# Optimization experiments

Hardware: AMD Instinct MI355X
Metric: run time of the kernel (lower is better)

The kernel has to match this reference:

```python
import jax, jax.numpy as jnp
import numpy as np

B, K, N = 8, 4, 131072
DENSITY = 0.3
NEG_PAD = -1000.0
NEG_IDLE = -1.0e8


def setup_inputs() -> dict:
    rng = np.random.default_rng(0)
    mask_s = rng.random((B, K, N)) < DENSITY  # bool, per-slot variable counts
    mask_a = rng.random((B, K, N)) < DENSITY
    ts = int(mask_s.sum())
    ta = int(mask_a.sum())
    key = jax.random.key(0)
    k1, k2, k3, k4 = jax.random.split(key, 4)
    return {
        "rgb": jax.random.normal(k1, (ts, 3), dtype=jnp.float32),
        "logits_surface": jax.random.normal(k2, (ts, 1), dtype=jnp.float32),
        "logits_air": jax.random.normal(k3, (ta, 1), dtype=jnp.float32),
        "idle_states": (jax.random.uniform(k4, (B, K)) < 0.25).astype(jnp.float32),
        "mask_eval_surface": jnp.asarray(mask_s),
        "mask_eval_air": jnp.asarray(mask_a),
    }


def _expand(mask, values):
    # mask: (B,K,N) bool; values: (total, C) packed in row-major (b,k,n) mask order.
    # Returns (B,K,N,C) where masked positions hold their packed value (others garbage,
    # to be overwritten by the caller's jnp.where). Equivalent to the torch B*K scatter loop.
    m = mask.reshape(-1)
    pos = jnp.cumsum(m.astype(jnp.int32)) - 1  # packed index for each masked slot
    pos = jnp.clip(pos, 0, values.shape[0] - 1)
    return jnp.take(values, pos, axis=0).reshape(mask.shape + (values.shape[-1],))


def reference(rgb, logits_surface, logits_air, idle_states,
              mask_eval_surface, mask_eval_air):
    alive = (1.0 - idle_states)[:, :, None, None]  # (B,K,1,1)
    idle = idle_states[:, :, None, None]
    ms = mask_eval_surface[..., None]  # (B,K,N,1)
    ma = mask_eval_air[..., None]

    rgb_out = jnp.where(ms, _expand(mask_eval_surface, rgb) * alive, 0.0)
    logits_surface_out = jnp.where(
        ms, _expand(mask_eval_surface, logits_surface) * alive + idle * NEG_IDLE, NEG_PAD)
    logits_air_out = jnp.where(
        ma, _expand(mask_eval_air, logits_air) * alive + idle * NEG_IDLE, NEG_PAD)
    return rgb_out, logits_surface_out, logits_air_out
```

## Files before the change

kernel.cpp:

```cpp
#include <hip/hip_runtime.h>
#include <stdint.h>

#define NTOT      4194304LL
#define CHUNK     2048
#define NBLK      2048
#define NEG_PAD   (-1000.0f)
#define NEG_IDLE  (-100000000.0f)
#define CAPS      832
#define CAPA      832

typedef unsigned long long u64;
typedef float float3u __attribute__((ext_vector_type(3), aligned(4)));
typedef float float4a __attribute__((ext_vector_type(4), aligned(16)));
typedef int   int4v   __attribute__((ext_vector_type(4), aligned(16)));

__global__ __launch_bounds__(256, 8) void count_kernel(
    const int* __restrict__ ms, const int* __restrict__ ma,
    unsigned short* __restrict__ cmp, u64* __restrict__ totals)
{
    const int t = threadIdx.x, lane = t & 63, wave = t >> 6;
    const unsigned bid = blockIdx.x;
    const long long base = (long long)bid * CHUNK;

    const int4v* ms4 = (const int4v*)(ms + base);
    const int4v* ma4 = (const int4v*)(ma + base);
    int4v s0 = __builtin_nontemporal_load(ms4 + 2 * t);
    int4v s1 = __builtin_nontemporal_load(ms4 + 2 * t + 1);
    int4v a0 = __builtin_nontemporal_load(ma4 + 2 * t);
    int4v a1 = __builtin_nontemporal_load(ma4 + 2 * t + 1);
    unsigned sbits = (unsigned)(s0[0] != 0)        | ((unsigned)(s0[1] != 0) << 1)
                   | ((unsigned)(s0[2] != 0) << 2) | ((unsigned)(s0[3] != 0) << 3)
                   | ((unsigned)(s1[0] != 0) << 4) | ((unsigned)(s1[1] != 0) << 5)
                   | ((unsigned)(s1[2] != 0) << 6) | ((unsigned)(s1[3] != 0) << 7);
    unsigned abits = (unsigned)(a0[0] != 0)        | ((unsigned)(a0[1] != 0) << 1)
                   | ((unsigned)(a0[2] != 0) << 2) | ((unsigned)(a0[3] != 0) << 3)
                   | ((unsigned)(a1[0] != 0) << 4) | ((unsigned)(a1[1] != 0) << 5)
                   | ((unsigned)(a1[2] != 0) << 6) | ((unsigned)(a1[3] != 0) << 7);

    cmp[bid * 256u + (unsigned)t] = (unsigned short)(sbits | (abits << 8));

    unsigned cnt = __popc(sbits) | (__popc(abits) << 16);
    #pragma unroll
    for (int o = 32; o; o >>= 1) cnt += __shfl_down(cnt, o, 64);
    __shared__ unsigned lds[4];
    if (lane == 0) lds[wave] = cnt;
    __syncthreads();
    if (t == 0) {
        unsigned tot = lds[0] + lds[1] + lds[2] + lds[3];
        totals[bid] = (u64)(tot & 0xffffu) | ((u64)(tot >> 16) << 32);
    }
}

__global__ __launch_bounds__(256, 5) void expand_kernel(
    const float* __restrict__ rgb, const float* __restrict__ lsurf,
    const float* __restrict__ lair, const float* __restrict__ idle,
    const unsigned short* __restrict__ cmp, const u64* __restrict__ totals,
    unsigned rgb_max, unsigned ts_max, unsigned ta_max,
    float* __restrict__ out_rgb, float* __restrict__ out_ls, float* __restrict__ out_la)
{
    __shared__ unsigned wsum[4];
    __shared__ u64 wacc[4];
    __shared__ unsigned packLDS[256];
    __shared__ unsigned prefLDS[256];
    __shared__ float    rgbLDS[3072];
    __shared__ float    rgbSrc[CAPS * 3];
    __shared__ float    lsS[CAPS];
    __shared__ float    laS[CAPA];

    const int t = threadIdx.x, lane = t & 63, wave = t >> 6;
    const unsigned bid = blockIdx.x;
    const long long base = (long long)bid * CHUNK;

    unsigned pk = cmp[bid * 256u + (unsigned)t];
    u64 acc = 0;
    #pragma unroll
    for (int j = 0; j < 8; ++j) {
        unsigned idx = (unsigned)t * 8u + (unsigned)j;
        acc += (idx < bid) ? totals[idx] : 0ULL;
    }
    const float idle_v = idle[(int)(base >> 17)];

    packLDS[t] = pk;
    unsigned cnt = __popc(pk & 0xffu) | (__popc(pk >> 8) << 16);

    unsigned x = cnt;
    #pragma unroll
    for (int o = 1; o < 64; o <<= 1) {
        unsigned y = __shfl_up(x, o, 64);
        if (lane >= o) x += y;
    }
    if (lane == 63) wsum[wave] = x;
    #pragma unroll
    for (int o = 32; o; o >>= 1) acc += __shfl_down(acc, o, 64);
    if (lane == 0) wacc[wave] = acc;
    __syncthreads();
    unsigned pre = (wave > 0 ? wsum[0] : 0u) + (wave > 1 ? wsum[1] : 0u)
                 + (wave > 2 ? wsum[2] : 0u);
    prefLDS[t] = pre + x - cnt;
    u64 basesum = wacc[0] + wacc[1] + wacc[2] + wacc[3];
    const unsigned excS = (unsigned)(basesum & 0xffffffffULL);
    const unsigned excA = (unsigned)(basesum >> 32);
    unsigned totPk = wsum[0] + wsum[1] + wsum[2] + wsum[3];
    const unsigned totS = totPk & 0xffffu;
    const unsigned totA = totPk >> 16;

    {
        const unsigned nS = totS < CAPS ? totS : CAPS;
        const unsigned nA = totA < CAPA ? totA : CAPA;
        const float* rgbB = rgb + 3LL * excS;
        const float* lsB  = lsurf + excS;
        const float* laB  = lair + excA;
        for (unsigned i = t; i < nS * 3u; i += 256u) rgbSrc[i] = rgbB[i];
        for (unsigned i = t; i < nS; i += 256u)      lsS[i]   = lsB[i];
        for (unsigned i = t; i < nA; i += 256u)      laS[i]   = laB[i];
    }
    __syncthreads();

    const float alive     = 1.0f - idle_v;
    const float idle_term = idle_v * NEG_IDLE;
    const int  sub = t >> 3, b = t & 7;
    const unsigned bm = (1u << b) - 1u;
    const int  hp = t >> 1;
    const unsigned nib = (unsigned)(t & 1) * 4u;
    const unsigned nm  = (1u << nib) - 1u;

    #pragma unroll
    for (int h = 0; h < 2; ++h) {
        #pragma unroll
        for (int r = 0; r < 4; ++r) {
            const int g = h * 4 + r;
            const int p = (g << 5) + sub;
            unsigned w  = packLDS[p];
            unsigned pv = prefLDS[p];
            const int li = r * 768 + 3 * t;
            if ((w >> b) & 1u) {
                unsigned lr = (pv & 0xffffu) + __popc(w & bm);
                float vx, vy, vz;
                if (lr < CAPS) {
                    vx = rgbSrc[3 * lr]; vy = rgbSrc[3 * lr + 1]; vz = rgbSrc[3 * lr + 2];
                } else {
                    unsigned pr = excS + lr; pr = pr < rgb_max ? pr : rgb_max;
                    float3u v = *(const float3u*)(rgb + 3LL * pr);
                    vx = v.x; vy = v.y; vz = v.z;
                }
                rgbLDS[li]     = vx * alive;
                rgbLDS[li + 1] = vy * alive;
                rgbLDS[li + 2] = vz * alive;
            } else {
                rgbLDS[li] = 0.f; rgbLDS[li + 1] = 0.f; rgbLDS[li + 2] = 0.f;
            }
        }
        {
            const int p = h * 128 + hp;
            unsigned w  = packLDS[p];
            unsigned pv = prefLDS[p];
            unsigned ws = w & 0xffu, wa = (w >> 8) & 0xffu;
            unsigned baseS = (pv & 0xffffu) + __popc(ws & nm);
            unsigned baseA = (pv >> 16)     + __popc(wa & nm);
            unsigned sb = (ws >> nib) & 0xFu;
            unsigned ab = (wa >> nib) & 0xFu;
            float lsv[4], lav[4];
            #pragma unroll
            for (int j = 0; j < 4; ++j) {
                unsigned mj = (1u << j) - 1u;
                unsigned rs = baseS + __popc(sb & mj);
                float vs = rs < CAPS ? lsS[rs]
                         : lsurf[(excS + rs) < ts_max ? (excS + rs) : ts_max];
                lsv[j] = ((sb >> j) & 1u) ? vs * alive + idle_term : NEG_PAD;
                unsigned ra = baseA + __popc(ab & mj);
                float va = ra < CAPA ? laS[ra]
                         : lair[(excA + ra) < ta_max ? (excA + ra) : ta_max];
                lav[j] = ((ab >> j) & 1u) ? va * alive + idle_term : NEG_PAD;
            }
            const long long eb = base + h * 1024 + 4 * t;
            float4a vls; vls.x = lsv[0]; vls.y = lsv[1]; vls.z = lsv[2]; vls.w = lsv[3];
            float4a vla; vla.x = lav[0]; vla.y = lav[1]; vla.z = lav[2]; vla.w = lav[3];
            __builtin_nontemporal_store(vls, (float4a*)(out_ls + eb));
            __builtin_nontemporal_store(vla, (float4a*)(out_la + eb));
        }
        __syncthreads();
        float4a* dst = (float4a*)(out_rgb + 3 * base) + h * 768;
        const float4a* src = (const float4a*)rgbLDS;
        __builtin_nontemporal_store(src[t],       dst + t);
        __builtin_nontemporal_store(src[t + 256], dst + t + 256);
        __builtin_nontemporal_store(src[t + 512], dst + t + 512);
        __syncthreads();
    }
}

extern "C" void kernel_launch(void* const* d_in, const int* in_sizes, int n_in,
                              void* d_out, int out_size, void* d_ws, size_t ws_size,
                              hipStream_t stream)
{
    const float* rgb   = (const float*)d_in[0];
    const float* lsurf = (const float*)d_in[1];
    const float* lair  = (const float*)d_in[2];
    const float* idle  = (const float*)d_in[3];
    const int*   ms    = (const int*)d_in[4];
    const int*   ma    = (const int*)d_in[5];

    unsigned rgb_max = (unsigned)(in_sizes[0] / 3 - 1);
    unsigned ts_max  = (unsigned)(in_sizes[1] - 1);
    unsigned ta_max  = (unsigned)(in_sizes[2] - 1);

    float* out     = (float*)d_out;
    float* out_rgb = out;
    float* out_ls  = out + NTOT * 3;
    float* out_la  = out_ls + NTOT;

    u64* totals = (u64*)d_ws;
    unsigned short* cmp = (unsigned short*)((char*)d_ws + 16384);

    count_kernel<<<NBLK, 256, 0, stream>>>(ms, ma, cmp, totals);
    expand_kernel<<<NBLK, 256, 0, stream>>>(rgb, lsurf, lair, idle, cmp, totals,
                                            rgb_max, ts_max, ta_max,
                                            out_rgb, out_ls, out_la);
}
```

Before: 150.0 us.

## Drop rgb LDS staging, vectorize aligned source loads, raise expand occupancy

Removes the rgbLDS transpose buffer and writes rgb outputs directly as strided scalar nontemporal stores, dropping two barriers per half. Source preloads into LDS now use aligned float4 nontemporal loads with head offset and tail handling. LDS caches shrink to 768 entries and launch bounds rise to 8 blocks per SM to improve occupancy. The trade-off is less coalesced rgb stores and more fallback global reads when a chunk exceeds the smaller cap.

```diff
diff --git a/kernel.cpp b/kernel.cpp
--- a/kernel.cpp
+++ b/kernel.cpp
@@ -6,8 +6,8 @@
 #define NBLK      2048
 #define NEG_PAD   (-1000.0f)
 #define NEG_IDLE  (-100000000.0f)
-#define CAPS      832
-#define CAPA      832
+#define CAPS      768
+#define CAPA      768
 
 typedef unsigned long long u64;
 typedef float float3u __attribute__((ext_vector_type(3), aligned(4)));
@@ -51,7 +51,7 @@
     }
 }
 
-__global__ __launch_bounds__(256, 5) void expand_kernel(
+__global__ __launch_bounds__(256, 8) void expand_kernel(
     const float* __restrict__ rgb, const float* __restrict__ lsurf,
     const float* __restrict__ lair, const float* __restrict__ idle,
     const unsigned short* __restrict__ cmp, const u64* __restrict__ totals,
@@ -62,10 +62,12 @@
     __shared__ u64 wacc[4];
     __shared__ unsigned packLDS[256];
     __shared__ unsigned prefLDS[256];
-    __shared__ float    rgbLDS[3072];
-    __shared__ float    rgbSrc[CAPS * 3];
-    __shared__ float    lsS[CAPS];
-    __shared__ float    laS[CAPA];
+    __shared__ float4a rgbSrc4[(CAPS * 3 + 4 + 3) / 4];
+    __shared__ float4a lsS4[(CAPS + 4 + 3) / 4];
+    __shared__ float4a laS4[(CAPA + 4 + 3) / 4];
+    float* const rgbSrc = (float*)rgbSrc4;
+    float* const lsS    = (float*)lsS4;
+    float* const laS    = (float*)laS4;
 
     const int t = threadIdx.x, lane = t & 63, wave = t >> 6;
     const unsigned bid = blockIdx.x;
@@ -104,15 +106,27 @@
     const unsigned totS = totPk & 0xffffu;
     const unsigned totA = totPk >> 16;
 
+    const unsigned nS = totS < CAPS ? totS : CAPS;
+    const unsigned nA = totA < CAPA ? totA : CAPA;
+    const unsigned ofsR = (excS * 3u) & 3u;
+    const unsigned ofsS = excS & 3u;
+    const unsigned ofsA = excA & 3u;
     {
-        const unsigned nS = totS < CAPS ? totS : CAPS;
-        const unsigned nA = totA < CAPA ? totA : CAPA;
-        const float* rgbB = rgb + 3LL * excS;
-        const float* lsB  = lsurf + excS;
-        const float* laB  = lair + excA;
-        for (unsigned i = t; i < nS * 3u; i += 256u) rgbSrc[i] = rgbB[i];
-        for (unsigned i = t; i < nS; i += 256u)      lsS[i]   = lsB[i];
-        for (unsigned i = t; i < nA; i += 256u)      laS[i]   = laB[i];
+        const unsigned FR = ofsR + nS * 3u, nvR = FR >> 2, tlR = FR & 3u;
+        const unsigned FS = ofsS + nS,      nvS = FS >> 2, tlS = FS & 3u;
+        const unsigned FA = ofsA + nA,      nvA = FA >> 2, tlA = FA & 3u;
+        const float4a* sR = (const float4a*)(rgb + (excS * 3u - ofsR));
+        const float4a* sS = (const float4a*)(lsurf + (excS - ofsS));
+        const float4a* sA = (const float4a*)(lair + (excA - ofsA));
+        for (unsigned i = t; i < nvR; i += 256u)
+            rgbSrc4[i] = __builtin_nontemporal_load(sR + i);
+        for (unsigned i = t; i < nvS; i += 256u)
+            lsS4[i] = __builtin_nontemporal_load(sS + i);
+        for (unsigned i = t; i < nvA; i += 256u)
+            laS4[i] = __builtin_nontemporal_load(sA + i);
+        if ((unsigned)t < tlR) rgbSrc[4u * nvR + t] = rgb[excS * 3u - ofsR + 4u * nvR + t];
+        if ((unsigned)t < tlS) lsS[4u * nvS + t]    = lsurf[excS - ofsS + 4u * nvS + t];
+        if ((unsigned)t < tlA) laS[4u * nvA + t]    = lair[excA - ofsA + 4u * nvA + t];
     }
     __syncthreads();
 
@@ -125,66 +139,58 @@
     const unsigned nm  = (1u << nib) - 1u;
 
     #pragma unroll
+    for (int g = 0; g < 8; ++g) {
+        const int p = (g << 5) + sub;
+        unsigned w  = packLDS[p];
+        unsigned pv = prefLDS[p];
+        const long long e = base + g * 256 + t;
+        float vx = 0.f, vy = 0.f, vz = 0.f;
+        if ((w >> b) & 1u) {
+            unsigned lr = (pv & 0xffffu) + __popc(w & bm);
+            if (lr < CAPS) {
+                vx = rgbSrc[ofsR + 3u * lr];
+                vy = rgbSrc[ofsR + 3u * lr + 1u];
+                vz = rgbSrc[ofsR + 3u * lr + 2u];
+            } else {
+                unsigned pr = excS + lr; pr = pr < rgb_max ? pr : rgb_max;
+                float3u v = *(const float3u*)(rgb + 3LL * pr);
+                vx = v.x; vy = v.y; vz = v.z;
+            }
+            vx *= alive; vy *= alive; vz *= alive;
+        }
+        __builtin_nontemporal_store(vx, out_rgb + 3 * e);
+        __builtin_nontemporal_store(vy, out_rgb + 3 * e + 1);
+        __builtin_nontemporal_store(vz, out_rgb + 3 * e + 2);
+    }
+
+    #pragma unroll
     for (int h = 0; h < 2; ++h) {
+        const int p = h * 128 + hp;
+        unsigned w  = packLDS[p];
+        unsigned pv = prefLDS[p];
+        unsigned ws = w & 0xffu, wa = (w >> 8) & 0xffu;
+        unsigned baseS = (pv & 0xffffu) + __popc(ws & nm);
+        unsigned baseA = (pv >> 16)     + __popc(wa & nm);
+        unsigned sb = (ws >> nib) & 0xFu;
+        unsigned ab = (wa >> nib) & 0xFu;
+        float lsv[4], lav[4];
         #pragma unroll
-        for (int r = 0; r < 4; ++r) {
-            const int g = h * 4 + r;
-            const int p = (g << 5) + sub;
-            unsigned w  = packLDS[p];
-            unsigned pv = prefLDS[p];
-            const int li = r * 768 + 3 * t;
-            if ((w >> b) & 1u) {
-                unsigned lr = (pv & 0xffffu) + __popc(w & bm);
-                float vx, vy, vz;
-                if (lr < CAPS) {
-                    vx = rgbSrc[3 * lr]; vy = rgbSrc[3 * lr + 1]; vz = rgbSrc[3 * lr + 2];
-                } else {
-                    unsigned pr = excS + lr; pr = pr < rgb_max ? pr : rgb_max;
-                    float3u v = *(const float3u*)(rgb + 3LL * pr);
-                    vx = v.x; vy = v.y; vz = v.z;
-                }
-                rgbLDS[li]     = vx * alive;
-                rgbLDS[li + 1] = vy * alive;
-                rgbLDS[li + 2] = vz * alive;
-            } else {
-                rgbLDS[li] = 0.f; rgbLDS[li + 1] = 0.f; rgbLDS[li + 2] = 0.f;
-            }
+        for (int j = 0; j < 4; ++j) {
+            unsigned mj = (1u << j) - 1u;
+            unsigned rs = baseS + __popc(sb & mj);
+            float vs = rs < CAPS ? lsS[ofsS + rs]
+                     : lsurf[(excS + rs) < ts_max ? (excS + rs) : ts_max];
+            lsv[j] = ((sb >> j) & 1u) ? vs * alive + idle_term : NEG_PAD;
+            unsigned ra = baseA + __popc(ab & mj);
+            float va = ra < CAPA ? laS[ofsA + ra]
+                     : lair[(excA + ra) < ta_max ? (excA + ra) : ta_max];
+            lav[j] = ((ab >> j) & 1u) ? va * alive + idle_term : NEG_PAD;
         }
-        {
-            const int p = h * 128 + hp;
-            unsigned w  = packLDS[p];
-            unsigned pv = prefLDS[p];
-            unsigned ws = w & 0xffu, wa = (w >> 8) & 0xffu;
-            unsigned baseS = (pv & 0xffffu) + __popc(ws & nm);
-            unsigned baseA = (pv >> 16)     + __popc(wa & nm);
-            unsigned sb = (ws >> nib) & 0xFu;
-            unsigned ab = (wa >> nib) & 0xFu;
-            float lsv[4], lav[4];
-            #pragma unroll
-            for (int j = 0; j < 4; ++j) {
-                unsigned mj = (1u << j) - 1u;
-                unsigned rs = baseS + __popc(sb & mj);
-                float vs = rs < CAPS ? lsS[rs]
-                         : lsurf[(excS + rs) < ts_max ? (excS + rs) : ts_max];
-                lsv[j] = ((sb >> j) & 1u) ? vs * alive + idle_term : NEG_PAD;
-                unsigned ra = baseA + __popc(ab & mj);
-                float va = ra < CAPA ? laS[ra]
-                         : lair[(excA + ra) < ta_max ? (excA + ra) : ta_max];
-                lav[j] = ((ab >> j) & 1u) ? va * alive + idle_term : NEG_PAD;
-            }
-            const long long eb = base + h * 1024 + 4 * t;
-            float4a vls; vls.x = lsv[0]; vls.y = lsv[1]; vls.z = lsv[2]; vls.w = lsv[3];
-            float4a vla; vla.x = lav[0]; vla.y = lav[1]; vla.z = lav[2]; vla.w = lav[3];
-            __builtin_nontemporal_store(vls, (float4a*)(out_ls + eb));
-            __builtin_nontemporal_store(vla, (float4a*)(out_la + eb));
-        }
-        __syncthreads();
-        float4a* dst = (float4a*)(out_rgb + 3 * base) + h * 768;
-        const float4a* src = (const float4a*)rgbLDS;
-        __builtin_nontemporal_store(src[t],       dst + t);
-        __builtin_nontemporal_store(src[t + 256], dst + t + 256);
-        __builtin_nontemporal_store(src[t + 512], dst + t + 512);
-        __syncthreads();
+        const long long eb = base + h * 1024 + 4 * t;
+        float4a vls; vls.x = lsv[0]; vls.y = lsv[1]; vls.z = lsv[2]; vls.w = lsv[3];
+        float4a vla; vla.x = lav[0]; vla.y = lav[1]; vla.z = lav[2]; vla.w = lav[3];
+        __builtin_nontemporal_store(vls, (float4a*)(out_ls + eb));
+        __builtin_nontemporal_store(vla, (float4a*)(out_la + eb));
     }
 }
 
```

Result: faster. 140.7 us (median of 2 runs) (-6.2%).
